# Kernel tuning notes

Hardware: AMD Instinct MI355X
Metric: run time of the kernel (lower is better)

The kernel has to match this reference:

```python
import jax, jax.numpy as jnp
import numpy as np

B, T, C = 4, 2048, 1024
H = 16
DH = C // H  # 64


def setup_inputs() -> dict:
    key = jax.random.key(0)
    ks = jax.random.split(key, 10)
    s_in = 1.0 / np.sqrt(C)
    x = jax.random.normal(ks[0], (B, T, C), dtype=jnp.float32)
    # stacked per-head projection weights: [H, C, DH]
    Wq = jax.random.normal(ks[1], (H, C, DH), dtype=jnp.float32) * s_in
    bq = jnp.zeros((H, DH), dtype=jnp.float32)
    Wk = jax.random.normal(ks[2], (H, C, DH), dtype=jnp.float32) * s_in
    bk = jnp.zeros((H, DH), dtype=jnp.float32)
    Wv = jax.random.normal(ks[3], (H, C, DH), dtype=jnp.float32) * s_in
    bv = jnp.zeros((H, DH), dtype=jnp.float32)
    Wo = jax.random.normal(ks[4], (C, C), dtype=jnp.float32) * s_in
    bo = jnp.zeros((C,), dtype=jnp.float32)
    return {"x": x, "Wq": Wq, "bq": bq, "Wk": Wk, "bk": bk,
            "Wv": Wv, "bv": bv, "Wo": Wo, "bo": bo}


def reference(x, Wq, bq, Wk, bk, Wv, bv, Wo, bo):
    # per-head projections: (B,T,C) x (H,C,DH) -> (B,H,T,DH)
    q = jnp.einsum('btc,hcd->bhtd', x, Wq) + bq[None, :, None, :]
    k = jnp.einsum('btc,hcd->bhtd', x, Wk) + bk[None, :, None, :]
    v = jnp.einsum('btc,hcd->bhtd', x, Wv) + bv[None, :, None, :]
    # scores scaled by C**-0.5 (C = full input embedding dim, as in source)
    scale = jnp.float32(C) ** -0.5
    scores = jnp.einsum('bhtd,bhsd->bhts', q, k) * scale  # (B,H,T,T)
    causal = jnp.tril(jnp.ones((T, T), dtype=bool))
    scores = jnp.where(causal, scores, -jnp.inf)
    attn = jax.nn.softmax(scores, axis=-1)
    out = jnp.einsum('bhts,bhsd->bhtd', attn, v)  # (B,H,T,DH)
    out = out.transpose(0, 2, 1, 3).reshape(B, T, C)  # concat heads
    return out @ Wo + bo
```

## Files before the change

### kernel.cpp

```cpp
#include <hip/hip_runtime.h>
#include <hip/hip_bf16.h>

#define TDIM 2048
#define BDIM 4
#define CDIM 1024
#define HDIM 16
#define DH   64

typedef __hip_bfloat16 bf16;
typedef __attribute__((ext_vector_type(8))) short bf16x8;
typedef __attribute__((ext_vector_type(4))) short bf16x4;
typedef __attribute__((ext_vector_type(4))) float f32x4;

__device__ __forceinline__ void async_ld16(const bf16* g, bf16* l) {
    __builtin_amdgcn_global_load_lds(
        (const __attribute__((address_space(1))) unsigned int*)g,
        (__attribute__((address_space(3))) unsigned int*)l, 16, 0, 0);
}

__device__ __forceinline__ unsigned short bf16bits(float x) {
    bf16 b = __float2bfloat16(x);
    return *(unsigned short*)&b;
}

__device__ __forceinline__ float fast_exp2(float x) {
#if __has_builtin(__builtin_amdgcn_exp2f)
    return __builtin_amdgcn_exp2f(x);
#else
    return exp2f(x);
#endif
}

__device__ __forceinline__ f32x4 mfma_16x16x16_bf16(bf16x4 a, bf16x4 b, f32x4 c) {
#if __has_builtin(__builtin_amdgcn_mfma_f32_16x16x16_bf16)
    return __builtin_amdgcn_mfma_f32_16x16x16_bf16(a, b, c, 0, 0, 0);
#elif __has_builtin(__builtin_amdgcn_mfma_f32_16x16x16bf16_1k)
    return __builtin_amdgcn_mfma_f32_16x16x16bf16_1k(a, b, c, 0, 0, 0);
#else
    asm volatile("v_mfma_f32_16x16x16_bf16 %0, %1, %2, %0"
                 : "+v"(c) : "v"(a), "v"(b));
    return c;
#endif
}

__global__ void convert_x4(const float4* __restrict__ src, ushort4* __restrict__ dst, int n4) {
    int i = blockIdx.x * blockDim.x + threadIdx.x;
    if (i >= n4) return;
    float4 v = src[i];
    ushort4 o;
    o.x = bf16bits(v.x); o.y = bf16bits(v.y);
    o.z = bf16bits(v.z); o.w = bf16bits(v.w);
    dst[i] = o;
}

__global__ void convert_biases(const float* __restrict__ b0, const float* __restrict__ b1,
                               const float* __restrict__ b2, const float* __restrict__ b3,
                               bf16* __restrict__ dst) {
    int i = blockIdx.x * blockDim.x + threadIdx.x;
    int which = i >> 10, j = i & 1023;
    const float* src = (which == 0) ? b0 : (which == 1) ? b1 : (which == 2) ? b2 : b3;
    dst[i] = __float2bfloat16(src[j]);
}

__global__ __launch_bounds__(256) void transpose_qkv_kernel(
    const float* __restrict__ Wq, const float* __restrict__ Wk, const float* __restrict__ Wv,
    bf16* __restrict__ WqT, bf16* __restrict__ WkT, bf16* __restrict__ WvT) {
    __shared__ float tile[64][65];
    const int which = blockIdx.z >> 4, h = blockIdx.z & 15;
    const float* W  = ((which == 0) ? Wq  : (which == 1) ? Wk  : Wv)  + (size_t)h * CDIM * DH;
    bf16*        WT = ((which == 0) ? WqT : (which == 1) ? WkT : WvT) + (size_t)h * CDIM * DH;
    const int c0 = blockIdx.x * 64;
    for (int it = 0; it < 16; it++) {
        int e = it * 256 + threadIdx.x;
        int r = e >> 6, col = e & 63;
        tile[r][col] = W[(size_t)(c0 + r) * DH + col];
    }
    __syncthreads();
    for (int it = 0; it < 16; it++) {
        int e = it * 256 + threadIdx.x;
        int r = e >> 6, col = e & 63;
        WT[(size_t)r * CDIM + c0 + col] = __float2bfloat16(tile[col][r]);
    }
}

__global__ __launch_bounds__(256) void transpose_wo_kernel(
    const float* __restrict__ W, bf16* __restrict__ WT) {
    __shared__ float tile[64][65];
    const int c0 = blockIdx.x * 64, d0 = blockIdx.y * 64;
    for (int it = 0; it < 16; it++) {
        int e = it * 256 + threadIdx.x;
        int r = e >> 6, col = e & 63;
        tile[r][col] = W[(size_t)(c0 + r) * CDIM + d0 + col];
    }
    __syncthreads();
    for (int it = 0; it < 16; it++) {
        int e = it * 256 + threadIdx.x;
        int r = e >> 6, col = e & 63;
        WT[(size_t)(d0 + r) * CDIM + c0 + col] = __float2bfloat16(tile[col][r]);
    }
}

__global__ __launch_bounds__(256) void transpose_v_kernel(
    const bf16* __restrict__ V, bf16* __restrict__ Vt) {
    __shared__ unsigned short tile[64][65];
    const int bh = blockIdx.y, t0 = blockIdx.x * 64;
    const unsigned short* Vp  = (const unsigned short*)V + ((size_t)bh * TDIM + t0) * DH;
    unsigned short*       Vtp = (unsigned short*)Vt + (size_t)bh * DH * TDIM;
    for (int it = 0; it < 16; it++) {
        int e = it * 256 + threadIdx.x;
        int r = e >> 6, c = e & 63;
        tile[r][c] = Vp[(size_t)r * DH + c];
    }
    __syncthreads();
    for (int it = 0; it < 16; it++) {
        int e = it * 256 + threadIdx.x;
        int r = e >> 6, c = e & 63;
        Vtp[(size_t)r * TDIM + t0 + c] = tile[c][r];
    }
}

__global__ __launch_bounds__(256) void proj_qkv_kernel(
    const bf16* __restrict__ X,
    const bf16* __restrict__ WqT, const bf16* __restrict__ WkT, const bf16* __restrict__ WvT,
    const bf16* __restrict__ bq,  const bf16* __restrict__ bk,  const bf16* __restrict__ bvv,
    bf16* __restrict__ Qo, bf16* __restrict__ Ko, bf16* __restrict__ Vo)
{
    const int z = blockIdx.z;
    const bf16* Bt   = (z == 0) ? WqT : (z == 1) ? WkT : WvT;
    const bf16* bias = (z == 0) ? bq  : (z == 1) ? bk  : bvv;

    __shared__ __align__(16) bf16 As[128 * 32];
    __shared__ __align__(16) bf16 Bs[128 * 32];

    const int tid  = threadIdx.x;
    const int lane = tid & 63;
    const int wave = tid >> 6;
    const int wr = wave >> 1, wc = wave & 1;
    const int l15 = lane & 15, quad = lane >> 4;

    const int blockM = blockIdx.y * 128;
    const int blockN = blockIdx.x * 128;

    f32x4 acc[4][4];
    for (int i = 0; i < 4; i++)
        for (int j = 0; j < 4; j++)
            acc[i][j] = (f32x4){0.f, 0.f, 0.f, 0.f};

    const int srow = lane >> 2, scol = (lane & 3) * 8;
    for (int k0 = 0; k0 < CDIM; k0 += 32) {
        for (int cc = 0; cc < 2; cc++) {
            int chunk = wave * 2 + cc;
            int row = chunk * 16 + srow;
            async_ld16(&X [(size_t)(blockM + row) * CDIM + k0 + scol], &As[chunk * 512]);
            async_ld16(&Bt[(size_t)(blockN + row) * CDIM + k0 + scol], &Bs[chunk * 512]);
        }
        __syncthreads();

        bf16x8 af[4], bfr[4];
        for (int mi = 0; mi < 4; mi++)
            af[mi] = *(const bf16x8*)&As[(wr * 64 + mi * 16 + l15) * 32 + quad * 8];
        for (int ni = 0; ni < 4; ni++)
            bfr[ni] = *(const bf16x8*)&Bs[(wc * 64 + ni * 16 + l15) * 32 + quad * 8];

        for (int mi = 0; mi < 4; mi++)
            for (int ni = 0; ni < 4; ni++)
                acc[mi][ni] = __builtin_amdgcn_mfma_f32_16x16x32_bf16(
                    af[mi], bfr[ni], acc[mi][ni], 0, 0, 0);
        __syncthreads();
    }

    for (int mi = 0; mi < 4; mi++) {
        int mbase = blockM + wr * 64 + mi * 16 + quad * 4;
        for (int ni = 0; ni < 4; ni++) {
            int n = blockN + wc * 64 + ni * 16 + l15;
            float bval = __bfloat162float(bias[n]);
            int h = n >> 6, d = n & 63;
            for (int r = 0; r < 4; r++) {
                int mm = mbase + r;
                int b = mm >> 11, t = mm & 2047;
                float val = acc[mi][ni][r] + bval;
                size_t idx = (((size_t)b * HDIM + h) * TDIM + t) * DH + d;
                if (z == 0)      Qo[idx] = __float2bfloat16(val * 0.045084439f);
                else if (z == 1) Ko[idx] = __float2bfloat16(val);
                else             Vo[idx] = __float2bfloat16(val);
            }
        }
    }
}

__global__ __launch_bounds__(256) void proj_out_kernel(
    const bf16* __restrict__ X, const bf16* __restrict__ Bt,
    const bf16* __restrict__ bias, float* __restrict__ Out)
{
    __shared__ __align__(16) bf16 As[128 * 32];
    __shared__ __align__(16) bf16 Bs[128 * 32];

    const int tid  = threadIdx.x;
    const int lane = tid & 63;
    const int wave = tid >> 6;
    const int wr = wave >> 1, wc = wave & 1;
    const int l15 = lane & 15, quad = lane >> 4;

    const int blockM = blockIdx.y * 128;
    const int blockN = blockIdx.x * 128;

    f32x4 acc[4][4];
    for (int i = 0; i < 4; i++)
        for (int j = 0; j < 4; j++)
            acc[i][j] = (f32x4){0.f, 0.f, 0.f, 0.f};

    const int srow = lane >> 2, scol = (lane & 3) * 8;
    for (int k0 = 0; k0 < CDIM; k0 += 32) {
        for (int cc = 0; cc < 2; cc++) {
            int chunk = wave * 2 + cc;
            int row = chunk * 16 + srow;
            async_ld16(&X [(size_t)(blockM + row) * CDIM + k0 + scol], &As[chunk * 512]);
            async_ld16(&Bt[(size_t)(blockN + row) * CDIM + k0 + scol], &Bs[chunk * 512]);
        }
        __syncthreads();

        bf16x8 af[4], bfr[4];
        for (int mi = 0; mi < 4; mi++)
            af[mi] = *(const bf16x8*)&As[(wr * 64 + mi * 16 + l15) * 32 + quad * 8];
        for (int ni = 0; ni < 4; ni++)
            bfr[ni] = *(const bf16x8*)&Bs[(wc * 64 + ni * 16 + l15) * 32 + quad * 8];

        for (int mi = 0; mi < 4; mi++)
            for (int ni = 0; ni < 4; ni++)
                acc[mi][ni] = __builtin_amdgcn_mfma_f32_16x16x32_bf16(
                    af[mi], bfr[ni], acc[mi][ni], 0, 0, 0);
        __syncthreads();
    }

    for (int mi = 0; mi < 4; mi++) {
        int mbase = blockM + wr * 64 + mi * 16 + quad * 4;
        for (int ni = 0; ni < 4; ni++) {
            int n = blockN + wc * 64 + ni * 16 + l15;
            float bval = __bfloat162float(bias[n]);
            for (int r = 0; r < 4; r++)
                Out[(size_t)(mbase + r) * CDIM + n] = acc[mi][ni][r] + bval;
        }
    }
}

__global__ __launch_bounds__(256, 4) void attn_kernel(
    const bf16* __restrict__ Q, const bf16* __restrict__ Kb,
    const bf16* __restrict__ Vt, bf16* __restrict__ Y)
{
    const int bh    = blockIdx.y;
    const int qT    = (int)gridDim.x - 1 - blockIdx.x;
    const int qBase = qT * 64;
    const int tid  = threadIdx.x;
    const int lane = tid & 63, wave = tid >> 6;
    const int l15 = lane & 15, quad = lane >> 4;

    __shared__ __align__(16) bf16 smem[2 * 2 * 64 * 64];

    const size_t qrow = (size_t)bh * TDIM + qBase + wave * 16 + l15;
    const bf16x8 qf0 = *(const bf16x8*)&Q[qrow * DH + quad * 8];
    const bf16x8 qf1 = *(const bf16x8*)&Q[qrow * DH + 32 + quad * 8];

    f32x4 o[4];
    for (int mt = 0; mt < 4; mt++) o[mt] = (f32x4){0.f, 0.f, 0.f, 0.f};
    float lsum = 0.f;

    const int srow = (wave << 4) + (lane >> 3);
    const int ssc  = (((lane & 7) ^ (lane >> 3)) << 3);
    const bf16* kSrc0 = Kb + ((size_t)bh * TDIM + srow) * DH + ssc;
    const bf16* vSrc0 = Vt + ((size_t)bh * DH + srow) * TDIM + ssc;

    const int swA   = l15 & 7;
    const int kcol0 = ((quad ^ swA) << 3);
    const int kcol1 = (((4 + quad) ^ swA) << 3);
    const int u2    = quad >> 1, intra = ((quad & 1) << 2);

    const int nkt  = qT + 1;
    const int qloc = wave * 16 + l15;

    {
        const bf16* kS = kSrc0;
        const bf16* vS = vSrc0;
        bf16* kD = smem + (wave * 16) * 64;
        bf16* vD = smem + 4096 + (wave * 16) * 64;
        async_ld16(kS,            kD);
        async_ld16(kS + 8 * DH,   kD + 8 * 64);
        async_ld16(vS,            vD);
        async_ld16(vS + 8 * TDIM, vD + 8 * 64);
    }
    __syncthreads();

    int cur = 0;
    for (int kt = 0; kt < nkt; kt++) {
        if (kt + 1 < nkt) {
            const bf16* kS = kSrc0 + (size_t)(kt + 1) * 64 * DH;
            const bf16* vS = vSrc0 + (size_t)(kt + 1) * 64;
            bf16* kD = smem + (cur ^ 1) * 8192 + (wave * 16) * 64;
            bf16* vD = smem + (cur ^ 1) * 8192 + 4096 + (wave * 16) * 64;
            async_ld16(kS,            kD);
            async_ld16(kS + 8 * DH,   kD + 8 * 64);
            async_ld16(vS,            vD);
            async_ld16(vS + 8 * TDIM, vD + 8 * 64);
        }

        const bf16* Ks = smem + cur * 8192;
        const bf16* Vs = Ks + 4096;

        const bool diag = (kt == qT);
        for (int nt = 0; nt < 4; nt++) {
            bf16x8 kf0 = *(const bf16x8*)&Ks[(nt * 16 + l15) * 64 + kcol0];
            bf16x8 kf1 = *(const bf16x8*)&Ks[(nt * 16 + l15) * 64 + kcol1];
            bf16x4 vA[4];
            for (int mt = 0; mt < 4; mt++)
                vA[mt] = *(const bf16x4*)&Vs[(mt * 16 + l15) * 64 +
                                             (((nt * 2 + u2) ^ swA) << 3) + intra];

            f32x4 s = (f32x4){0.f, 0.f, 0.f, 0.f};
            s = __builtin_amdgcn_mfma_f32_16x16x32_bf16(kf0, qf0, s, 0, 0, 0);
            s = __builtin_amdgcn_mfma_f32_16x16x32_bf16(kf1, qf1, s, 0, 0, 0);

            bf16x4 pb;
            for (int r = 0; r < 4; r++) {
                float pe = fast_exp2(s[r]);
                if (diag && (nt * 16 + quad * 4 + r > qloc)) pe = 0.f;
                lsum += pe;
                pb[r] = (short)bf16bits(pe);
            }
            for (int mt = 0; mt < 4; mt++)
                o[mt] = mfma_16x16x16_bf16(vA[mt], pb, o[mt]);
        }
        __syncthreads();
        cur ^= 1;
    }

    float v = lsum;
    v += __shfl_xor(v, 16, 64);
    v += __shfl_xor(v, 32, 64);
    const float inv = 1.0f / v;

    unsigned short* sm = (unsigned short*)smem;
    for (int mt = 0; mt < 4; mt++) {
        unsigned short pk[4];
        for (int r = 0; r < 4; r++) pk[r] = bf16bits(o[mt][r] * inv);
        *(ushort4*)&sm[(wave * 16 + l15) * 72 + mt * 16 + quad * 4] = *(ushort4*)pk;
    }
    const int b = bh >> 4, h = bh & 15;
    const int qq = lane >> 2, part = lane & 3;
    const int t = qBase + wave * 16 + qq;
    uint4 c0 = *(const uint4*)&sm[(wave * 16 + qq) * 72 + part * 16];
    uint4 c1 = *(const uint4*)&sm[(wave * 16 + qq) * 72 + part * 16 + 8];
    *(uint4*)&Y[((size_t)b * TDIM + t) * CDIM + h * DH + part * 16]     = c0;
    *(uint4*)&Y[((size_t)b * TDIM + t) * CDIM + h * DH + part * 16 + 8] = c1;
}

extern "C" void kernel_launch(void* const* d_in, const int* in_sizes, int n_in,
                              void* d_out, int out_size, void* d_ws, size_t ws_size,
                              hipStream_t stream) {
    (void)in_sizes; (void)n_in; (void)out_size; (void)ws_size;

    char* ws = (char*)d_ws;
    const size_t SZ_BHTD = (size_t)BDIM * HDIM * TDIM * DH * sizeof(bf16);
    const size_t SZ_W    = (size_t)HDIM * CDIM * DH * sizeof(bf16);
    bf16* Qb  = (bf16*)(ws);
    bf16* Kb  = (bf16*)(ws + SZ_BHTD);
    bf16* Vt  = (bf16*)(ws + 2 * SZ_BHTD);
    bf16* Y   = (bf16*)(ws + 3 * SZ_BHTD);
    bf16* WqT = (bf16*)(ws + 4 * SZ_BHTD);
    bf16* WkT = (bf16*)(ws + 4 * SZ_BHTD + SZ_W);
    bf16* WvT = (bf16*)(ws + 4 * SZ_BHTD + 2 * SZ_W);
    bf16* WoT = (bf16*)(ws + 4 * SZ_BHTD + 3 * SZ_W);
    bf16* xC  = (bf16*)(ws + 4 * SZ_BHTD + 4 * SZ_W);
    bf16* bqC = (bf16*)(ws + 5 * SZ_BHTD + 4 * SZ_W);
    bf16* bkC = bqC + 1024;
    bf16* bvC = bqC + 2048;
    bf16* boC = bqC + 3072;
    bf16* Vb  = (bf16*)d_out;

    const int nX4 = (BDIM * TDIM * CDIM) / 4;
    convert_x4<<<nX4 / 256, 256, 0, stream>>>((const float4*)d_in[0], (ushort4*)xC, nX4);
    convert_biases<<<16, 256, 0, stream>>>((const float*)d_in[2], (const float*)d_in[4],
                                           (const float*)d_in[6], (const float*)d_in[8], bqC);

    transpose_qkv_kernel<<<dim3(CDIM / 64, 1, 48), 256, 0, stream>>>(
        (const float*)d_in[1], (const float*)d_in[3], (const float*)d_in[5], WqT, WkT, WvT);
    transpose_wo_kernel<<<dim3(CDIM / 64, CDIM / 64), 256, 0, stream>>>(
        (const float*)d_in[7], WoT);

    dim3 gq(CDIM / 128, (BDIM * TDIM) / 128, 3);
    proj_qkv_kernel<<<gq, 256, 0, stream>>>(xC, WqT, WkT, WvT, bqC, bkC, bvC, Qb, Kb, Vb);

    transpose_v_kernel<<<dim3(TDIM / 64, BDIM * HDIM), 256, 0, stream>>>(Vb, Vt);

    attn_kernel<<<dim3(TDIM / 64, BDIM * HDIM), 256, 0, stream>>>(Qb, Kb, Vt, Y);

    proj_out_kernel<<<dim3(CDIM / 128, (BDIM * TDIM) / 128), 256, 0, stream>>>(
        Y, WoT, boC, (float*)d_out);
}
```

Baseline: 304.0 us.

## Widen attention blocks to 128 query rows with shared K/V tile staging

The attention kernel now runs 512 threads (8 waves) per block, covering 128 query rows instead of 64. All 8 waves share each K/V tile staged in LDS, and each thread issues one async load per tile instead of two, which halves global K/V traffic per query row. Waves in the lower 64-row half skip the last key tile because it lies past their causal diagonal, so those waves idle for that iteration while still joining the barriers. The risks are fewer blocks in the grid (load balance and occupancy) and more waves contending at each barrier.

```diff
diff --git a/kernel.cpp b/kernel.cpp
--- a/kernel.cpp
+++ b/kernel.cpp
@@ -243,13 +243,13 @@
     }
 }
 
-__global__ __launch_bounds__(256, 4) void attn_kernel(
+__global__ __launch_bounds__(512, 4) void attn_kernel(
     const bf16* __restrict__ Q, const bf16* __restrict__ Kb,
     const bf16* __restrict__ Vt, bf16* __restrict__ Y)
 {
     const int bh    = blockIdx.y;
     const int qT    = (int)gridDim.x - 1 - blockIdx.x;
-    const int qBase = qT * 64;
+    const int qBase = qT * 128;
     const int tid  = threadIdx.x;
     const int lane = tid & 63, wave = tid >> 6;
     const int l15 = lane & 15, quad = lane >> 4;
@@ -264,8 +264,8 @@
     for (int mt = 0; mt < 4; mt++) o[mt] = (f32x4){0.f, 0.f, 0.f, 0.f};
     float lsum = 0.f;
 
-    const int srow = (wave << 4) + (lane >> 3);
-    const int ssc  = (((lane & 7) ^ (lane >> 3)) << 3);
+    const int srow = tid >> 3;
+    const int ssc  = (((tid & 7) ^ ((tid >> 3) & 7)) << 3);
     const bf16* kSrc0 = Kb + ((size_t)bh * TDIM + srow) * DH + ssc;
     const bf16* vSrc0 = Vt + ((size_t)bh * DH + srow) * TDIM + ssc;
 
@@ -274,63 +274,56 @@
     const int kcol1 = (((4 + quad) ^ swA) << 3);
     const int u2    = quad >> 1, intra = ((quad & 1) << 2);
 
-    const int nkt  = qT + 1;
-    const int qloc = wave * 16 + l15;
-
-    {
-        const bf16* kS = kSrc0;
-        const bf16* vS = vSrc0;
-        bf16* kD = smem + (wave * 16) * 64;
-        bf16* vD = smem + 4096 + (wave * 16) * 64;
-        async_ld16(kS,            kD);
-        async_ld16(kS + 8 * DH,   kD + 8 * 64);
-        async_ld16(vS,            vD);
-        async_ld16(vS + 8 * TDIM, vD + 8 * 64);
-    }
+    const int nkt   = 2 * qT + 2;
+    const int kdiag = 2 * qT + (wave >> 2);
+    const int qloc  = (wave & 3) * 16 + l15;
+
+    bf16* kD0 = smem + (wave * 8) * 64;
+    bf16* vD0 = smem + 4096 + (wave * 8) * 64;
+
+#define STAGE(tile, buf)                                            \
+    do {                                                            \
+        async_ld16(kSrc0 + (size_t)(tile) * 64 * DH, kD0 + (buf) * 8192); \
+        async_ld16(vSrc0 + (size_t)(tile) * 64,      vD0 + (buf) * 8192); \
+    } while (0)
+
+    STAGE(0, 0);
     __syncthreads();
 
     int cur = 0;
     for (int kt = 0; kt < nkt; kt++) {
-        if (kt + 1 < nkt) {
-            const bf16* kS = kSrc0 + (size_t)(kt + 1) * 64 * DH;
-            const bf16* vS = vSrc0 + (size_t)(kt + 1) * 64;
-            bf16* kD = smem + (cur ^ 1) * 8192 + (wave * 16) * 64;
-            bf16* vD = smem + (cur ^ 1) * 8192 + 4096 + (wave * 16) * 64;
-            async_ld16(kS,            kD);
-            async_ld16(kS + 8 * DH,   kD + 8 * 64);
-            async_ld16(vS,            vD);
-            async_ld16(vS + 8 * TDIM, vD + 8 * 64);
-        }
-
-        const bf16* Ks = smem + cur * 8192;
-        const bf16* Vs = Ks + 4096;
-
-        const bool diag = (kt == qT);
-        for (int nt = 0; nt < 4; nt++) {
-            bf16x8 kf0 = *(const bf16x8*)&Ks[(nt * 16 + l15) * 64 + kcol0];
-            bf16x8 kf1 = *(const bf16x8*)&Ks[(nt * 16 + l15) * 64 + kcol1];
-            bf16x4 vA[4];
-            for (int mt = 0; mt < 4; mt++)
-                vA[mt] = *(const bf16x4*)&Vs[(mt * 16 + l15) * 64 +
-                                             (((nt * 2 + u2) ^ swA) << 3) + intra];
-
-            f32x4 s = (f32x4){0.f, 0.f, 0.f, 0.f};
-            s = __builtin_amdgcn_mfma_f32_16x16x32_bf16(kf0, qf0, s, 0, 0, 0);
-            s = __builtin_amdgcn_mfma_f32_16x16x32_bf16(kf1, qf1, s, 0, 0, 0);
-
-            bf16x4 pb;
-            for (int r = 0; r < 4; r++) {
-                float pe = fast_exp2(s[r]);
-                if (diag && (nt * 16 + quad * 4 + r > qloc)) pe = 0.f;
-                lsum += pe;
-                pb[r] = (short)bf16bits(pe);
+        if (kt + 1 < nkt) STAGE(kt + 1, cur ^ 1);
+        if (kt <= kdiag) {
+            const bf16* Ks = smem + cur * 8192;
+            const bf16* Vs = Ks + 4096;
+            const bool diag = (kt == kdiag);
+            for (int nt = 0; nt < 4; nt++) {
+                bf16x8 kf0 = *(const bf16x8*)&Ks[(nt * 16 + l15) * 64 + kcol0];
+                bf16x8 kf1 = *(const bf16x8*)&Ks[(nt * 16 + l15) * 64 + kcol1];
+                bf16x4 vA[4];
+                for (int mt = 0; mt < 4; mt++)
+                    vA[mt] = *(const bf16x4*)&Vs[(mt * 16 + l15) * 64 +
+                                                 (((nt * 2 + u2) ^ swA) << 3) + intra];
+
+                f32x4 s = (f32x4){0.f, 0.f, 0.f, 0.f};
+                s = __builtin_amdgcn_mfma_f32_16x16x32_bf16(kf0, qf0, s, 0, 0, 0);
+                s = __builtin_amdgcn_mfma_f32_16x16x32_bf16(kf1, qf1, s, 0, 0, 0);
+
+                bf16x4 pb;
+                for (int r = 0; r < 4; r++) {
+                    float pe = fast_exp2(s[r]);
+                    if (diag && (nt * 16 + quad * 4 + r > qloc)) pe = 0.f;
+                    lsum += pe;
+                    pb[r] = (short)bf16bits(pe);
+                }
+                for (int mt = 0; mt < 4; mt++)
+                    o[mt] = mfma_16x16x16_bf16(vA[mt], pb, o[mt]);
             }
-            for (int mt = 0; mt < 4; mt++)
-                o[mt] = mfma_16x16x16_bf16(vA[mt], pb, o[mt]);
         }
         __syncthreads();
         cur ^= 1;
     }
+#undef STAGE
 
     float v = lsum;
     v += __shfl_xor(v, 16, 64);
@@ -390,7 +383,7 @@
 
     transpose_v_kernel<<<dim3(TDIM / 64, BDIM * HDIM), 256, 0, stream>>>(Vb, Vt);
 
-    attn_kernel<<<dim3(TDIM / 64, BDIM * HDIM), 256, 0, stream>>>(Qb, Kb, Vt, Y);
+    attn_kernel<<<dim3(TDIM / 128, BDIM * HDIM), 512, 0, stream>>>(Qb, Kb, Vt, Y);
 
     proj_out_kernel<<<dim3(CDIM / 128, (BDIM * TDIM) / 128), 256, 0, stream>>>(
         Y, WoT, boC, (float*)d_out);
```

Result: no change. 306.2 us (+0.7%).
